# Optimization experiments

Measured on AMD Instinct MI355X. Metric: run time of the kernel, lower is better.

Reference implementation:

```python
import jax, jax.numpy as jnp
import numpy as np

DIM = 32
ED = DIM * DIM          # 1024
HID = ED * 4            # 4096
EPS = 1e-5


def _ln(x, g, b):
    # LayerNorm over last two dims (d, d)
    m = x.mean(axis=(-2, -1), keepdims=True)
    v = jnp.var(x, axis=(-2, -1), keepdims=True)
    return (x - m) * jax.lax.rsqrt(v + EPS) * g + b


def setup_inputs() -> dict:
    key = jax.random.key(0)
    ks = jax.random.split(key, 10)
    b, s, d = 2, 1024, DIM
    inp = {
        "x": jax.random.normal(ks[0], (b, s, d, d), dtype=jnp.float32),
        # StateSpaceLayer params
        "log_A": jax.random.normal(ks[1], (d,), dtype=jnp.float32) * 0.02,
        "w_dt": jax.random.normal(ks[2], (d,), dtype=jnp.float32) / np.sqrt(d),
        "b_dt": jnp.zeros((), dtype=jnp.float32),
        "g_ssm": jnp.ones((d, d), dtype=jnp.float32),
        "b_ssm": jnp.zeros((d, d), dtype=jnp.float32),
        # FFN params
        "g_ffn": jnp.ones((d, d), dtype=jnp.float32),
        "b_ffn": jnp.zeros((d, d), dtype=jnp.float32),
        "W1": jax.random.normal(ks[3], (ED, HID), dtype=jnp.float32) / np.sqrt(ED),
        "bb1": jnp.zeros((HID,), dtype=jnp.float32),
        "W2": jax.random.normal(ks[4], (HID, ED), dtype=jnp.float32) / np.sqrt(HID),
        "bb2": jnp.zeros((ED,), dtype=jnp.float32),
    }
    return inp


def reference(x, log_A, w_dt, b_dt, g_ssm, b_ssm, g_ffn, b_ffn, W1, bb1, W2, bb2):
    b, s, d, _ = x.shape
    # ---- StateSpaceLayer (parallel / training path) ----
    xn = _ln(x, g_ssm, b_ssm)                          # (b,s,d,d)
    A_cont = -jnp.exp(log_A)                           # (d,)
    # dt_proj: Linear(d,1) over last axis, then squeeze -> (b,s,d)
    dt = jax.nn.softplus(jnp.einsum('bsrc,c->bsr', xn, w_dt) + b_dt)
    log_a = dt * A_cont                                # (b,s,d)
    cs = jnp.cumsum(log_a, axis=1)                     # (b,s,d)
    log_M = cs[:, :, None, :] - cs[:, None, :, :]      # (b,t,j,d)
    tmask = jnp.arange(s)[:, None] >= jnp.arange(s)[None, :]  # (t,j) causal
    M = jnp.where(tmask[None, :, :, None], jnp.exp(log_M), 0.0)
    ssm_out = jnp.einsum('btjr,bjrc->btrc', M, xn) + x  # residual
    # ---- MatrixFeedForward ----
    fn = _ln(ssm_out, g_ffn, b_ffn).reshape(b, s, d * d)
    h = jax.nn.gelu(fn @ W1 + bb1, approximate=False)
    y = (h @ W2 + bb2).reshape(b, s, d, d)
    return ssm_out + y
```

## Files before the change

kernel.cpp:

```cpp
#include <hip/hip_runtime.h>
#include <math.h>

#define EPSF 1e-5f

typedef __attribute__((ext_vector_type(4))) float f32x4;
typedef __attribute__((ext_vector_type(4))) int i32x4;
typedef __attribute__((ext_vector_type(8))) int i32x8;

__device__ __forceinline__ unsigned short f2bf(float f) {
  unsigned int u = __float_as_uint(f);
  u += 0x7FFFu + ((u >> 16) & 1u);
  return (unsigned short)(u >> 16);
}
__device__ __forceinline__ float bf2f(unsigned short u) {
  return __uint_as_float((unsigned int)u << 16);
}

__device__ __forceinline__ void async_load16(const void* g, void* l) {
  __builtin_amdgcn_global_load_lds(
      (const __attribute__((address_space(1))) void*)g,
      (__attribute__((address_space(3))) void*)l, 16, 0, 0);
}


__global__ __launch_bounds__(256) void k_pre(
    const float* __restrict__ x, const float* __restrict__ g, const float* __restrict__ bta,
    const float* __restrict__ w_dt, const float* __restrict__ b_dt,
    const float* __restrict__ log_A, unsigned short* __restrict__ xn, float* __restrict__ log_a,
    const float* __restrict__ W1, unsigned char* __restrict__ W1t,
    const float* __restrict__ W2, unsigned char* __restrict__ W2t) {
  __shared__ float smem[64 * 65];
  int tid = threadIdx.x;
  if (blockIdx.x < 2048) {
    int bs = blockIdx.x;
    int t = tid;
    float4 v = ((const float4*)(x + (size_t)bs * 1024))[t];
    float s = v.x + v.y + v.z + v.w;
    float ss = v.x * v.x + v.y * v.y + v.z * v.z + v.w * v.w;
    #pragma unroll
    for (int o = 1; o < 64; o <<= 1) { s += __shfl_xor(s, o); ss += __shfl_xor(ss, o); }
    float* red = smem;
    int w = t >> 6;
    if ((t & 63) == 0) { red[w] = s; red[4 + w] = ss; }
    __syncthreads();
    float S = red[0] + red[1] + red[2] + red[3];
    float SS = red[4] + red[5] + red[6] + red[7];
    float m = S * (1.0f / 1024.0f);
    float var = SS * (1.0f / 1024.0f) - m * m;
    float inv = rsqrtf(var + EPSF);
    float4 gv = ((const float4*)g)[t];
    float4 bv = ((const float4*)bta)[t];
    float4 o;
    o.x = (v.x - m) * inv * gv.x + bv.x;
    o.y = (v.y - m) * inv * gv.y + bv.y;
    o.z = (v.z - m) * inv * gv.z + bv.z;
    o.w = (v.w - m) * inv * gv.w + bv.w;
    ushort4 ob;
    ob.x = f2bf(o.x); ob.y = f2bf(o.y); ob.z = f2bf(o.z); ob.w = f2bf(o.w);
    ((ushort4*)(xn + (size_t)bs * 1024))[t] = ob;
    float4 wv = ((const float4*)w_dt)[t & 7];
    float part = o.x * wv.x + o.y * wv.y + o.z * wv.z + o.w * wv.w;
    part += __shfl_xor(part, 1);
    part += __shfl_xor(part, 2);
    part += __shfl_xor(part, 4);
    if ((t & 7) == 0) {
      int r = t >> 3;
      float z = part + b_dt[0];
      float sp = (z > 20.0f) ? z : log1pf(expf(z));
      log_a[(size_t)bs * 32 + r] = sp * (-expf(log_A[r]));
    }
  } else {
    int bid = blockIdx.x - 2048;
    bool isW1 = bid < 1024;
    const float* src; unsigned char* dst; int C, r0, c0, NK;
    if (isW1) { src = W1; dst = W1t; C = 4096; NK = 8;
                c0 = (bid & 63) * 64; r0 = (bid >> 6) * 64; }
    else { bid -= 1024; src = W2; dst = W2t; C = 1024; NK = 32;
           c0 = (bid & 15) * 64; r0 = (bid >> 4) * 64; }
    #pragma unroll
    for (int q = 0; q < 4; ++q) {
      int lin = q * 256 + tid;
      int r = lin >> 4, cq = lin & 15;
      float4 v = *(const float4*)(src + (size_t)(r0 + r) * C + c0 + cq * 4);
      smem[r * 65 + cq * 4 + 0] = v.x; smem[r * 65 + cq * 4 + 1] = v.y;
      smem[r * 65 + cq * 4 + 2] = v.z; smem[r * 65 + cq * 4 + 3] = v.w;
    }
    __syncthreads();
    #pragma unroll
    for (int q = 0; q < 2; ++q) {
      int lin = q * 256 + tid;
      int c = lin & 63, rh = lin >> 6;
      int n = c0 + c, k = r0 + rh * 8;
      int p0 = __builtin_amdgcn_cvt_pk_fp8_f32(
          smem[(rh * 8 + 0) * 65 + c] * 16.0f, smem[(rh * 8 + 1) * 65 + c] * 16.0f, 0, false);
      p0 = __builtin_amdgcn_cvt_pk_fp8_f32(
          smem[(rh * 8 + 2) * 65 + c] * 16.0f, smem[(rh * 8 + 3) * 65 + c] * 16.0f, p0, true);
      int p1 = __builtin_amdgcn_cvt_pk_fp8_f32(
          smem[(rh * 8 + 4) * 65 + c] * 16.0f, smem[(rh * 8 + 5) * 65 + c] * 16.0f, 0, false);
      p1 = __builtin_amdgcn_cvt_pk_fp8_f32(
          smem[(rh * 8 + 6) * 65 + c] * 16.0f, smem[(rh * 8 + 7) * 65 + c] * 16.0f, p1, true);
      int2 pk; pk.x = p0; pk.y = p1;
      size_t sb = (size_t)(n >> 4) * NK + (k >> 7);
      int l = ((k >> 5) & 3) * 16 + (n & 15);
      *(int2*)(dst + sb * 2048 + ((k >> 4) & 1) * 1024 + l * 16 + (k & 15)) = pk;
    }
  }
}

template <int PASS>
__global__ __launch_bounds__(256) void k_scan_pass(
    const unsigned short* __restrict__ xn, const float* __restrict__ x,
    const float* __restrict__ loga, float4* __restrict__ E, float* __restrict__ P,
    const float* __restrict__ bb2, float* __restrict__ out) {
  int bx = blockIdx.x;
  int b = bx >> 8, r = (bx >> 3) & 31, ch = bx & 7;
  int tid = threadIdx.x, cg = tid & 7, sub = tid >> 3;
  __shared__ float dec[128];
  __shared__ float4 sE[32][8];
  __shared__ float sP[32];
  if (tid < 128)
    dec[tid] = expf(loga[(size_t)(b * 1024 + ch * 128 + tid) * 32 + r]);
  __syncthreads();
  int t0 = ch * 128 + sub * 4;
  size_t base = ((size_t)(b * 1024 + t0) * 1024 + r * 32 + cg * 4) >> 2;
  const ushort4* xn4 = (const ushort4*)xn;
  float4 xv[4];
  #pragma unroll
  for (int i = 0; i < 4; ++i) {
    ushort4 u = xn4[base + (size_t)i * 256];
    xv[i].x = bf2f(u.x); xv[i].y = bf2f(u.y); xv[i].z = bf2f(u.z); xv[i].w = bf2f(u.w);
  }
  float4 S = {0.f, 0.f, 0.f, 0.f};
  float Pl = 1.0f;
  #pragma unroll
  for (int i = 0; i < 4; ++i) {
    float d = dec[sub * 4 + i];
    S.x = d * S.x + xv[i].x; S.y = d * S.y + xv[i].y;
    S.z = d * S.z + xv[i].z; S.w = d * S.w + xv[i].w;
    Pl *= d;
  }
  sE[sub][cg] = S;
  if (cg == 0) sP[sub] = Pl;
  __syncthreads();
  if (PASS == 0) {
    if (tid < 8) {
      float4 Et = {0.f, 0.f, 0.f, 0.f};
      float PP = 1.0f;
      #pragma unroll
      for (int h = 0; h < 32; ++h) {
        float p = sP[h]; float4 e = sE[h][tid];
        Et.x = p * Et.x + e.x; Et.y = p * Et.y + e.y;
        Et.z = p * Et.z + e.z; Et.w = p * Et.w + e.w;
        PP *= p;
      }
      E[((size_t)(b * 32 + r) * 8 + ch) * 8 + tid] = Et;
      if (tid == 0) P[(b * 32 + r) * 8 + ch] = PP;
    }
  } else {
    float4 Sin = {0.f, 0.f, 0.f, 0.f};
    const float4* Eb = E + (size_t)(b * 32 + r) * 64 + cg;
    const float* Pb = P + (size_t)(b * 32 + r) * 8;
    for (int h = 0; h < ch; ++h) {
      float p = Pb[h]; float4 e = Eb[h * 8];
      Sin.x = p * Sin.x + e.x; Sin.y = p * Sin.y + e.y;
      Sin.z = p * Sin.z + e.z; Sin.w = p * Sin.w + e.w;
    }
    for (int h = 0; h < sub; ++h) {
      float p = sP[h]; float4 e = sE[h][cg];
      Sin.x = p * Sin.x + e.x; Sin.y = p * Sin.y + e.y;
      Sin.z = p * Sin.z + e.z; Sin.w = p * Sin.w + e.w;
    }
    float4 bb = ((const float4*)bb2)[r * 8 + cg];
    const float4* x4 = (const float4*)x;
    float4* out4 = (float4*)out;
    #pragma unroll
    for (int i = 0; i < 4; ++i) {
      float d = dec[sub * 4 + i];
      Sin.x = d * Sin.x + xv[i].x; Sin.y = d * Sin.y + xv[i].y;
      Sin.z = d * Sin.z + xv[i].z; Sin.w = d * Sin.w + xv[i].w;
      float4 rx = x4[base + (size_t)i * 256];
      float4 oi;
      oi.x = Sin.x + rx.x + bb.x; oi.y = Sin.y + rx.y + bb.y;
      oi.z = Sin.z + rx.z + bb.z; oi.w = Sin.w + rx.w + bb.w;
      out4[base + (size_t)i * 256] = oi;
    }
  }
}

__global__ __launch_bounds__(256) void k_ln2(
    const float* __restrict__ out, const float* __restrict__ bb2,
    const float* __restrict__ g, const float* __restrict__ bta,
    unsigned char* __restrict__ fn) {
  int bs = blockIdx.x;
  int t = threadIdx.x;
  float4 v = ((const float4*)(out + (size_t)bs * 1024))[t];
  float4 bb = ((const float4*)bb2)[t];
  v.x -= bb.x; v.y -= bb.y; v.z -= bb.z; v.w -= bb.w;
  float s = v.x + v.y + v.z + v.w;
  float ss = v.x * v.x + v.y * v.y + v.z * v.z + v.w * v.w;
  #pragma unroll
  for (int o = 1; o < 64; o <<= 1) { s += __shfl_xor(s, o); ss += __shfl_xor(ss, o); }
  __shared__ float red[8];
  int w = t >> 6;
  if ((t & 63) == 0) { red[w] = s; red[4 + w] = ss; }
  __syncthreads();
  float S = red[0] + red[1] + red[2] + red[3];
  float SS = red[4] + red[5] + red[6] + red[7];
  float m = S * (1.0f / 1024.0f);
  float var = SS * (1.0f / 1024.0f) - m * m;
  float inv = rsqrtf(var + EPSF);
  float4 gv = ((const float4*)g)[t];
  float4 bv = ((const float4*)bta)[t];
  float f0 = (v.x - m) * inv * gv.x + bv.x;
  float f1 = (v.y - m) * inv * gv.y + bv.y;
  float f2 = (v.z - m) * inv * gv.z + bv.z;
  float f3 = (v.w - m) * inv * gv.w + bv.w;
  int p = __builtin_amdgcn_cvt_pk_fp8_f32(f0, f1, 0, false);
  p = __builtin_amdgcn_cvt_pk_fp8_f32(f2, f3, p, true);
  int k = t * 4;
  size_t sb = (size_t)(bs >> 4) * 8 + (k >> 7);
  int l = ((k >> 5) & 3) * 16 + (bs & 15);
  *(int*)(fn + sb * 2048 + ((k >> 4) & 1) * 1024 + l * 16 + (k & 15)) = p;
}

template <int EPI, int NK>
__global__ __launch_bounds__(256, 2) void k_gemm_lds(
    const unsigned char* __restrict__ Ap, const unsigned char* __restrict__ Bp,
    const float* __restrict__ bias, void* __restrict__ C) {
  __shared__ __align__(16) unsigned char sAB[65536];
  unsigned char* sA = sAB;
  unsigned char* sB = sAB + 32768;
  int L = blockIdx.x;
  int m0, n0, kp0;
  if (EPI == 0) {
    int xcd = L & 7;
    int nq = xcd & 3, mh = xcd >> 2;
    int rest = L >> 3;
    int nx = rest & 7, my = rest >> 3;
    n0 = (nq * 8 + nx) * 128;
    m0 = (mh * 8 + my) * 128;
    kp0 = 0;
  } else {
    int xcd = L & 7;
    int ks = xcd >> 1, mh = xcd & 1;
    int rest = L >> 3;
    int nx = rest & 7, my = rest >> 3;
    n0 = nx * 128;
    m0 = (mh * 8 + my) * 128;
    kp0 = ks * 8;
  }
  int tid = threadIdx.x;
  int wave = tid >> 6, lane = tid & 63;
  int wr = wave >> 1, wc = wave & 1;
  int l15 = lane & 15, quad = lane >> 4;
  int mt0b = m0 >> 4, nt0b = n0 >> 4;

  f32x4 zero = {0.0f, 0.0f, 0.0f, 0.0f};
  f32x4 acc[4][4];
  #pragma unroll
  for (int i = 0; i < 4; ++i)
    #pragma unroll
    for (int j = 0; j < 4; ++j) acc[i][j] = zero;

  const unsigned char* gsrc = (wave < 2) ? Ap : Bp;
  int rt0 = (wave < 2) ? mt0b : nt0b;
  unsigned char* ldsb = (wave < 2) ? sA : sB;
  int w01 = wave & 1;

  #pragma unroll 1
  for (int st = 0; st < 4; ++st) {
    int kpb = kp0 + st * 2;
    #pragma unroll
    for (int t = 0; t < 16; ++t) {
      int s = w01 * 8 + (t >> 1);
      int h = t & 1;
      int rt = s >> 1, kt = s & 1;
      async_load16(gsrc + ((size_t)(rt0 + rt) * NK + (kpb + kt)) * 2048 + h * 1024 + lane * 16,
                   ldsb + s * 2048 + h * 1024 + lane * 16);
    }
    __syncthreads();
    #pragma unroll
    for (int kl = 0; kl < 2; ++kl) {
      i32x8 af[4], bf[4];
      #pragma unroll
      for (int i = 0; i < 4; ++i) {
        const unsigned char* pa = sA + ((wr * 4 + i) * 2 + kl) * 2048 + lane * 16;
        i32x4 lo = *(const i32x4*)pa;
        i32x4 hi = *(const i32x4*)(pa + 1024);
        af[i] = __builtin_shufflevector(lo, hi, 0, 1, 2, 3, 4, 5, 6, 7);
      }
      #pragma unroll
      for (int j = 0; j < 4; ++j) {
        const unsigned char* pb = sB + ((wc * 4 + j) * 2 + kl) * 2048 + lane * 16;
        i32x4 lo = *(const i32x4*)pb;
        i32x4 hi = *(const i32x4*)(pb + 1024);
        bf[j] = __builtin_shufflevector(lo, hi, 0, 1, 2, 3, 4, 5, 6, 7);
      }
      #pragma unroll
      for (int i = 0; i < 4; ++i)
        #pragma unroll
        for (int j = 0; j < 4; ++j)
          acc[i][j] = __builtin_amdgcn_mfma_scale_f32_16x16x128_f8f6f4(
              af[i], bf[j], acc[i][j], 0, 0, 0, 0x7F7F7F7F, 0, 0x7F7F7F7F);
    }
    __syncthreads();
  }

  if (EPI == 0) {
    unsigned char* sC = sAB;
    #pragma unroll
    for (int i = 0; i < 4; ++i) {
      #pragma unroll
      for (int j = 0; j < 4; ++j) {
        int col_l = wc * 64 + j * 16 + l15;
        float bval = bias[n0 + col_l];
        int half2 = (col_l >> 4) & 1, lb = (col_l >> 5) & 3;
        unsigned char* ld = sC + (wr * 4 + i) * 2048 + half2 * 1024 +
                            (lb * 16 + quad * 4) * 16 + l15;
        float vv[4];
        #pragma unroll
        for (int v = 0; v < 4; ++v) {
          float val = acc[i][j][v] * 0.0625f + bval;
          vv[v] = 0.5f * val * (1.0f + erff(val * 0.70710678118654752f));
        }
        int p01 = __builtin_amdgcn_cvt_pk_fp8_f32(vv[0], vv[1], 0, false);
        int p23 = __builtin_amdgcn_cvt_pk_fp8_f32(vv[2], vv[3], 0, false);
        ld[0 * 16] = (unsigned char)(p01 & 0xff);
        ld[1 * 16] = (unsigned char)((p01 >> 8) & 0xff);
        ld[2 * 16] = (unsigned char)(p23 & 0xff);
        ld[3 * 16] = (unsigned char)((p23 >> 8) & 0xff);
      }
    }
    __syncthreads();
    unsigned char* C8 = (unsigned char*)C;
    int mt2_0 = m0 >> 4, kp2 = n0 >> 7;
    #pragma unroll
    for (int p = 0; p < 4; ++p) {
      int ci = p * 256 + tid;
      int s = ci >> 7, off = (ci & 127) * 16;
      *(int4*)(C8 + ((size_t)(mt2_0 + s) * 32 + kp2) * 2048 + off) =
          *(const int4*)(sC + s * 2048 + off);
    }
  } else {
    float* O = (float*)C;
    #pragma unroll
    for (int i = 0; i < 4; ++i)
      #pragma unroll
      for (int j = 0; j < 4; ++j) {
        int col = n0 + wc * 64 + j * 16 + l15;
        #pragma unroll
        for (int v = 0; v < 4; ++v) {
          int row = m0 + wr * 64 + i * 16 + quad * 4 + v;
          atomicAdd(&O[(size_t)row * 1024 + col], acc[i][j][v] * 0.0625f);
        }
      }
  }
}

extern "C" void kernel_launch(void* const* d_in, const int* in_sizes, int n_in,
                              void* d_out, int out_size, void* d_ws, size_t ws_size,
                              hipStream_t stream) {
  const float* x     = (const float*)d_in[0];
  const float* log_A = (const float*)d_in[1];
  const float* w_dt  = (const float*)d_in[2];
  const float* b_dt  = (const float*)d_in[3];
  const float* g_ssm = (const float*)d_in[4];
  const float* b_ssm = (const float*)d_in[5];
  const float* g_ffn = (const float*)d_in[6];
  const float* b_ffn = (const float*)d_in[7];
  const float* W1    = (const float*)d_in[8];
  const float* bb1   = (const float*)d_in[9];
  const float* W2    = (const float*)d_in[10];
  const float* bb2   = (const float*)d_in[11];
  float* out = (float*)d_out;

  const size_t MB = 1u << 20;
  char* ws = (char*)d_ws;
  unsigned short* xn   = (unsigned short*)(ws);
  unsigned char* W1t   = (unsigned char*)(ws + 4 * MB);
  float* loga          = (float*)(ws + 8 * MB);
  float4* Ebuf         = (float4*)(ws + 8 * MB + 262144);
  float* Pbuf          = (float*)(ws + 8 * MB + 393216);
  unsigned char* fn    = (unsigned char*)(ws + 9 * MB);
  unsigned char* W2t   = (unsigned char*)(ws + 11 * MB);
  unsigned char* hbf   = (unsigned char*)(ws + 15 * MB);

  k_pre<<<4096, 256, 0, stream>>>(x, g_ssm, b_ssm, w_dt, b_dt, log_A, xn, loga,
                                  W1, W1t, W2, W2t);
  k_scan_pass<0><<<512, 256, 0, stream>>>(xn, x, loga, Ebuf, Pbuf, bb2, out);
  k_scan_pass<1><<<512, 256, 0, stream>>>(xn, x, loga, Ebuf, Pbuf, bb2, out);
  k_ln2<<<2048, 256, 0, stream>>>(out, bb2, g_ffn, b_ffn, fn);
  k_gemm_lds<0, 8><<<512, 256, 0, stream>>>(fn, W1t, bb1, (void*)hbf);
  k_gemm_lds<1, 32><<<512, 256, 0, stream>>>(hbf, W2t, nullptr, (void*)out);
}
```

Before: 171.0 us.

## Double-buffer GEMM LDS loads and replace split-K atomics with 64x64 tiles

Splits the templated GEMM into two kernels that both prefetch the next K-slice into a second LDS buffer while the MFMAs run on the current one, using vmcnt waits and raw barriers. The second GEMM drops the 4-way split-K with atomicAdd and instead uses 64x64 output tiles over the full K range, with a plain read-modify-write to add into the output. This removes atomic traffic and exposed load latency, at the cost of longer per-block K loops and lower MFMA work per LDS fetch in GEMM2.

```diff
diff --git a/kernel.cpp b/kernel.cpp
--- a/kernel.cpp
+++ b/kernel.cpp
@@ -223,37 +223,21 @@
   *(int*)(fn + sb * 2048 + ((k >> 4) & 1) * 1024 + l * 16 + (k & 15)) = p;
 }
 
-template <int EPI, int NK>
-__global__ __launch_bounds__(256, 2) void k_gemm_lds(
+__global__ __launch_bounds__(256, 2) void k_gemm1(
     const unsigned char* __restrict__ Ap, const unsigned char* __restrict__ Bp,
-    const float* __restrict__ bias, void* __restrict__ C) {
+    const float* __restrict__ bias, unsigned char* __restrict__ C8) {
   __shared__ __align__(16) unsigned char sAB[65536];
-  unsigned char* sA = sAB;
-  unsigned char* sB = sAB + 32768;
   int L = blockIdx.x;
-  int m0, n0, kp0;
-  if (EPI == 0) {
-    int xcd = L & 7;
-    int nq = xcd & 3, mh = xcd >> 2;
-    int rest = L >> 3;
-    int nx = rest & 7, my = rest >> 3;
-    n0 = (nq * 8 + nx) * 128;
-    m0 = (mh * 8 + my) * 128;
-    kp0 = 0;
-  } else {
-    int xcd = L & 7;
-    int ks = xcd >> 1, mh = xcd & 1;
-    int rest = L >> 3;
-    int nx = rest & 7, my = rest >> 3;
-    n0 = nx * 128;
-    m0 = (mh * 8 + my) * 128;
-    kp0 = ks * 8;
-  }
+  int xcd = L & 7;
+  int nq = xcd & 3, mh = xcd >> 2;
+  int rest = L >> 3;
+  int nx = rest & 7, my = rest >> 3;
+  int n0 = (nq * 8 + nx) * 128;
+  int m0 = (mh * 8 + my) * 128;
   int tid = threadIdx.x;
   int wave = tid >> 6, lane = tid & 63;
   int wr = wave >> 1, wc = wave & 1;
   int l15 = lane & 15, quad = lane >> 4;
-  int mt0b = m0 >> 4, nt0b = n0 >> 4;
 
   f32x4 zero = {0.0f, 0.0f, 0.0f, 0.0f};
   f32x4 acc[4][4];
@@ -263,98 +247,190 @@
     for (int j = 0; j < 4; ++j) acc[i][j] = zero;
 
   const unsigned char* gsrc = (wave < 2) ? Ap : Bp;
-  int rt0 = (wave < 2) ? mt0b : nt0b;
-  unsigned char* ldsb = (wave < 2) ? sA : sB;
+  int rt0 = (wave < 2) ? (m0 >> 4) : (n0 >> 4);
+  int aoff = (wave < 2) ? 0 : 16384;
   int w01 = wave & 1;
 
+  #pragma unroll
+  for (int t = 0; t < 8; ++t) {
+    int idx = w01 * 8 + t, rt = idx >> 1, h = idx & 1;
+    async_load16(gsrc + ((size_t)(rt0 + rt) * 8 + 0) * 2048 + h * 1024 + lane * 16,
+                 sAB + aoff + rt * 2048 + h * 1024 + lane * 16);
+  }
+
   #pragma unroll 1
-  for (int st = 0; st < 4; ++st) {
-    int kpb = kp0 + st * 2;
-    #pragma unroll
-    for (int t = 0; t < 16; ++t) {
-      int s = w01 * 8 + (t >> 1);
-      int h = t & 1;
-      int rt = s >> 1, kt = s & 1;
-      async_load16(gsrc + ((size_t)(rt0 + rt) * NK + (kpb + kt)) * 2048 + h * 1024 + lane * 16,
-                   ldsb + s * 2048 + h * 1024 + lane * 16);
-    }
-    __syncthreads();
+  for (int st = 0; st < 8; ++st) {
+    int cur = (st & 1) * 32768;
+    if (st < 7) {
+      int nxt = cur ^ 32768;
+      #pragma unroll
+      for (int t = 0; t < 8; ++t) {
+        int idx = w01 * 8 + t, rt = idx >> 1, h = idx & 1;
+        async_load16(gsrc + ((size_t)(rt0 + rt) * 8 + st + 1) * 2048 + h * 1024 + lane * 16,
+                     sAB + nxt + aoff + rt * 2048 + h * 1024 + lane * 16);
+      }
+      asm volatile("s_waitcnt vmcnt(8)" ::: "memory");
+    } else {
+      asm volatile("s_waitcnt vmcnt(0)" ::: "memory");
+    }
+    __builtin_amdgcn_s_barrier();
+    const unsigned char* sA = sAB + cur;
+    const unsigned char* sB = sAB + cur + 16384;
+    i32x8 af[4], bf[4];
+    #pragma unroll
+    for (int i = 0; i < 4; ++i) {
+      const unsigned char* pa = sA + (wr * 4 + i) * 2048 + lane * 16;
+      i32x4 lo = *(const i32x4*)pa;
+      i32x4 hi = *(const i32x4*)(pa + 1024);
+      af[i] = __builtin_shufflevector(lo, hi, 0, 1, 2, 3, 4, 5, 6, 7);
+    }
+    #pragma unroll
+    for (int j = 0; j < 4; ++j) {
+      const unsigned char* pb = sB + (wc * 4 + j) * 2048 + lane * 16;
+      i32x4 lo = *(const i32x4*)pb;
+      i32x4 hi = *(const i32x4*)(pb + 1024);
+      bf[j] = __builtin_shufflevector(lo, hi, 0, 1, 2, 3, 4, 5, 6, 7);
+    }
+    #pragma unroll
+    for (int i = 0; i < 4; ++i)
+      #pragma unroll
+      for (int j = 0; j < 4; ++j)
+        acc[i][j] = __builtin_amdgcn_mfma_scale_f32_16x16x128_f8f6f4(
+            af[i], bf[j], acc[i][j], 0, 0, 0, 0x7F7F7F7F, 0, 0x7F7F7F7F);
+    asm volatile("s_waitcnt lgkmcnt(0)" ::: "memory");
+    __builtin_amdgcn_s_barrier();
+  }
+
+  unsigned char* sC = sAB;
+  #pragma unroll
+  for (int i = 0; i < 4; ++i) {
+    #pragma unroll
+    for (int j = 0; j < 4; ++j) {
+      int col_l = wc * 64 + j * 16 + l15;
+      float bval = bias[n0 + col_l];
+      int half2 = (col_l >> 4) & 1, lb = (col_l >> 5) & 3;
+      unsigned char* ld = sC + (wr * 4 + i) * 2048 + half2 * 1024 +
+                          (lb * 16 + quad * 4) * 16 + l15;
+      float vv[4];
+      #pragma unroll
+      for (int v = 0; v < 4; ++v) {
+        float val = acc[i][j][v] * 0.0625f + bval;
+        vv[v] = 0.5f * val * (1.0f + erff(val * 0.70710678118654752f));
+      }
+      int p01 = __builtin_amdgcn_cvt_pk_fp8_f32(vv[0], vv[1], 0, false);
+      int p23 = __builtin_amdgcn_cvt_pk_fp8_f32(vv[2], vv[3], 0, false);
+      ld[0 * 16] = (unsigned char)(p01 & 0xff);
+      ld[1 * 16] = (unsigned char)((p01 >> 8) & 0xff);
+      ld[2 * 16] = (unsigned char)(p23 & 0xff);
+      ld[3 * 16] = (unsigned char)((p23 >> 8) & 0xff);
+    }
+  }
+  __syncthreads();
+  int mt2_0 = m0 >> 4, kp2 = n0 >> 7;
+  #pragma unroll
+  for (int p = 0; p < 4; ++p) {
+    int ci = p * 256 + tid;
+    int s = ci >> 7, off = (ci & 127) * 16;
+    *(int4*)(C8 + ((size_t)(mt2_0 + s) * 32 + kp2) * 2048 + off) =
+        *(const int4*)(sC + s * 2048 + off);
+  }
+}
+
+__global__ __launch_bounds__(256, 2) void k_gemm2(
+    const unsigned char* __restrict__ Ap, const unsigned char* __restrict__ Bp,
+    float* __restrict__ O) {
+  __shared__ __align__(16) unsigned char sAB[65536];
+  int L = blockIdx.x;
+  int xcd = L & 7;
+  int rest = L >> 3;
+  int nl = rest & 1, mt = rest >> 1;
+  int n0 = (xcd * 2 + nl) * 64;
+  int m0 = mt * 64;
+  int tid = threadIdx.x;
+  int wave = tid >> 6, lane = tid & 63;
+  int wr = wave >> 1, wc = wave & 1;
+  int l15 = lane & 15, quad = lane >> 4;
+
+  f32x4 zero = {0.0f, 0.0f, 0.0f, 0.0f};
+  f32x4 acc[2][2];
+  #pragma unroll
+  for (int i = 0; i < 2; ++i)
+    #pragma unroll
+    for (int j = 0; j < 2; ++j) acc[i][j] = zero;
+
+  const unsigned char* gsrc = (wave < 2) ? Ap : Bp;
+  int rt0 = (wave < 2) ? (m0 >> 4) : (n0 >> 4);
+  int aoff = (wave < 2) ? 0 : 16384;
+  int w01 = wave & 1;
+
+  #pragma unroll
+  for (int t = 0; t < 8; ++t) {
+    int idx = w01 * 8 + t, sb = idx >> 1, h = idx & 1;
+    int rt = sb >> 1, kt = sb & 1;
+    async_load16(gsrc + ((size_t)(rt0 + rt) * 32 + kt) * 2048 + h * 1024 + lane * 16,
+                 sAB + aoff + sb * 2048 + h * 1024 + lane * 16);
+  }
+
+  #pragma unroll 1
+  for (int st = 0; st < 16; ++st) {
+    int cur = (st & 1) * 32768;
+    if (st < 15) {
+      int nxt = cur ^ 32768;
+      #pragma unroll
+      for (int t = 0; t < 8; ++t) {
+        int idx = w01 * 8 + t, sb = idx >> 1, h = idx & 1;
+        int rt = sb >> 1, kt = sb & 1;
+        async_load16(
+            gsrc + ((size_t)(rt0 + rt) * 32 + (st + 1) * 2 + kt) * 2048 + h * 1024 + lane * 16,
+            sAB + nxt + aoff + sb * 2048 + h * 1024 + lane * 16);
+      }
+      asm volatile("s_waitcnt vmcnt(8)" ::: "memory");
+    } else {
+      asm volatile("s_waitcnt vmcnt(0)" ::: "memory");
+    }
+    __builtin_amdgcn_s_barrier();
+    const unsigned char* sA = sAB + cur;
+    const unsigned char* sB = sAB + cur + 16384;
     #pragma unroll
     for (int kl = 0; kl < 2; ++kl) {
-      i32x8 af[4], bf[4];
-      #pragma unroll
-      for (int i = 0; i < 4; ++i) {
-        const unsigned char* pa = sA + ((wr * 4 + i) * 2 + kl) * 2048 + lane * 16;
+      i32x8 af[2], bf[2];
+      #pragma unroll
+      for (int i = 0; i < 2; ++i) {
+        const unsigned char* pa = sA + ((wr * 2 + i) * 2 + kl) * 2048 + lane * 16;
         i32x4 lo = *(const i32x4*)pa;
         i32x4 hi = *(const i32x4*)(pa + 1024);
         af[i] = __builtin_shufflevector(lo, hi, 0, 1, 2, 3, 4, 5, 6, 7);
       }
       #pragma unroll
-      for (int j = 0; j < 4; ++j) {
-        const unsigned char* pb = sB + ((wc * 4 + j) * 2 + kl) * 2048 + lane * 16;
+      for (int j = 0; j < 2; ++j) {
+        const unsigned char* pb = sB + ((wc * 2 + j) * 2 + kl) * 2048 + lane * 16;
         i32x4 lo = *(const i32x4*)pb;
         i32x4 hi = *(const i32x4*)(pb + 1024);
         bf[j] = __builtin_shufflevector(lo, hi, 0, 1, 2, 3, 4, 5, 6, 7);
       }
       #pragma unroll
-      for (int i = 0; i < 4; ++i)
+      for (int i = 0; i < 2; ++i)
         #pragma unroll
-        for (int j = 0; j < 4; ++j)
+        for (int j = 0; j < 2; ++j)
           acc[i][j] = __builtin_amdgcn_mfma_scale_f32_16x16x128_f8f6f4(
               af[i], bf[j], acc[i][j], 0, 0, 0, 0x7F7F7F7F, 0, 0x7F7F7F7F);
     }
-    __syncthreads();
-  }
-
-  if (EPI == 0) {
-    unsigned char* sC = sAB;
-    #pragma unroll
-    for (int i = 0; i < 4; ++i) {
-      #pragma unroll
-      for (int j = 0; j < 4; ++j) {
-        int col_l = wc * 64 + j * 16 + l15;
-        float bval = bias[n0 + col_l];
-        int half2 = (col_l >> 4) & 1, lb = (col_l >> 5) & 3;
-        unsigned char* ld = sC + (wr * 4 + i) * 2048 + half2 * 1024 +
-                            (lb * 16 + quad * 4) * 16 + l15;
-        float vv[4];
-        #pragma unroll
-        for (int v = 0; v < 4; ++v) {
-          float val = acc[i][j][v] * 0.0625f + bval;
-          vv[v] = 0.5f * val * (1.0f + erff(val * 0.70710678118654752f));
-        }
-        int p01 = __builtin_amdgcn_cvt_pk_fp8_f32(vv[0], vv[1], 0, false);
-        int p23 = __builtin_amdgcn_cvt_pk_fp8_f32(vv[2], vv[3], 0, false);
-        ld[0 * 16] = (unsigned char)(p01 & 0xff);
-        ld[1 * 16] = (unsigned char)((p01 >> 8) & 0xff);
-        ld[2 * 16] = (unsigned char)(p23 & 0xff);
-        ld[3 * 16] = (unsigned char)((p23 >> 8) & 0xff);
-      }
-    }
-    __syncthreads();
-    unsigned char* C8 = (unsigned char*)C;
-    int mt2_0 = m0 >> 4, kp2 = n0 >> 7;
-    #pragma unroll
-    for (int p = 0; p < 4; ++p) {
-      int ci = p * 256 + tid;
-      int s = ci >> 7, off = (ci & 127) * 16;
-      *(int4*)(C8 + ((size_t)(mt2_0 + s) * 32 + kp2) * 2048 + off) =
-          *(const int4*)(sC + s * 2048 + off);
-    }
-  } else {
-    float* O = (float*)C;
-    #pragma unroll
-    for (int i = 0; i < 4; ++i)
-      #pragma unroll
-      for (int j = 0; j < 4; ++j) {
-        int col = n0 + wc * 64 + j * 16 + l15;
-        #pragma unroll
-        for (int v = 0; v < 4; ++v) {
-          int row = m0 + wr * 64 + i * 16 + quad * 4 + v;
-          atomicAdd(&O[(size_t)row * 1024 + col], acc[i][j][v] * 0.0625f);
-        }
-      }
-  }
+    asm volatile("s_waitcnt lgkmcnt(0)" ::: "memory");
+    __builtin_amdgcn_s_barrier();
+  }
+
+  #pragma unroll
+  for (int i = 0; i < 2; ++i)
+    #pragma unroll
+    for (int j = 0; j < 2; ++j) {
+      int col = n0 + wc * 32 + j * 16 + l15;
+      #pragma unroll
+      for (int v = 0; v < 4; ++v) {
+        int row = m0 + wr * 32 + i * 16 + quad * 4 + v;
+        float* p = &O[(size_t)row * 1024 + col];
+        *p = *p + acc[i][j][v] * 0.0625f;
+      }
+    }
 }
 
 extern "C" void kernel_launch(void* const* d_in, const int* in_sizes, int n_in,
@@ -390,6 +466,6 @@
   k_scan_pass<0><<<512, 256, 0, stream>>>(xn, x, loga, Ebuf, Pbuf, bb2, out);
   k_scan_pass<1><<<512, 256, 0, stream>>>(xn, x, loga, Ebuf, Pbuf, bb2, out);
   k_ln2<<<2048, 256, 0, stream>>>(out, bb2, g_ffn, b_ffn, fn);
-  k_gemm_lds<0, 8><<<512, 256, 0, stream>>>(fn, W1t, bb1, (void*)hbf);
-  k_gemm_lds<1, 32><<<512, 256, 0, stream>>>(hbf, W2t, nullptr, (void*)out);
-}
+  k_gemm1<<<512, 256, 0, stream>>>(fn, W1t, bb1, hbf);
+  k_gemm2<<<512, 256, 0, stream>>>(hbf, W2t, out);
+}
```

Measured after the change: 154.2 us. -9.8%, faster.
